# Kernel optimization log

Measured on AMD Instinct MI355X. Metric: run time of the kernel, lower is better.

Reference implementation:

```python
import jax, jax.numpy as jnp
import numpy as np

B, S, P, G, E = 16, 1024, 32, 64, 512
HD = E // 2          # head_dim = 256
SCALE = HD ** -0.5
LAMBDA_INIT = 0.8 - 0.6 * float(np.exp(-0.3 * 0.0))  # depth=0 -> 0.2
EPS = 1e-5


def setup_inputs() -> dict:
    key = jax.random.key(0)
    ks = jax.random.split(key, 12)
    inp = {
        'query': jax.random.normal(ks[0], (B, S, E), jnp.float32),
        'key': jax.random.normal(ks[1], (B, P, G, E), jnp.float32),
        'mask': jax.random.randint(ks[2], (B, S), 0, 2).astype(bool),
        'Wq': jax.random.normal(ks[3], (E, E), jnp.float32) * (E ** -0.5),
        'Wk': jax.random.normal(ks[4], (E, E), jnp.float32) * (E ** -0.5),
        'Wv': jax.random.normal(ks[5], (E, E), jnp.float32) * (E ** -0.5),
        'Wo': jax.random.normal(ks[6], (E, E), jnp.float32) * (E ** -0.5),
        'lq1': jax.random.normal(ks[7], (HD,), jnp.float32) * 0.1,
        'lk1': jax.random.normal(ks[8], (HD,), jnp.float32) * 0.1,
        'lq2': jax.random.normal(ks[9], (HD,), jnp.float32) * 0.1,
        'lk2': jax.random.normal(ks[10], (HD,), jnp.float32) * 0.1,
        'gamma': jnp.ones((E,), jnp.float32),
    }
    return inp


def reference(query, key, mask, Wq, Wk, Wv, Wo, lq1, lk1, lq2, lk2, gamma):
    b, s, e = query.shape
    _, p, g, _ = key.shape
    L = p * g
    key2d = key.reshape(b, L, e)

    Q = (query @ Wq).reshape(b, s, 2, HD).transpose(0, 2, 1, 3) * SCALE  # [B,2,S,hd]
    K = (key2d @ Wk).reshape(b, L, 2, HD).transpose(0, 2, 1, 3)          # [B,2,L,hd]
    V = key2d @ Wv                                                       # [B,L,E]

    scores = jnp.einsum('bhsd,bhld->bhsl', Q, K)                         # [B,2,S,L]
    # masked_fill(~mask, 0.0) with mask broadcast [B,1,S,1]
    scores = jnp.where(mask[:, None, :, None], scores, 0.0)
    attn = jax.nn.softmax(scores, axis=-1)

    lam1 = jnp.exp(jnp.sum(lq1 * lk1))
    lam2 = jnp.exp(jnp.sum(lq2 * lk2))
    lam = lam1 - lam2 + LAMBDA_INIT

    diff = attn[:, 0] - lam * attn[:, 1]                                 # [B,S,L]
    out2d = jnp.einsum('bsl,ble->bse', diff, V)                          # [B,S,E]

    # RMSNorm over last dim with affine gamma
    rms = out2d * jax.lax.rsqrt(jnp.mean(out2d * out2d, axis=-1, keepdims=True) + EPS)
    rms = rms * gamma
    out = (rms * (1.0 - LAMBDA_INIT)) @ Wo                               # [B,S,E]

    return out, diff.reshape(b, s, p, g)
```

## Files before the change

### kernel.cpp

```cpp
#include <hip/hip_runtime.h>
#include <hip/hip_bf16.h>


typedef short short8 __attribute__((ext_vector_type(8)));
typedef __bf16 bf16x8 __attribute__((ext_vector_type(8)));
typedef float f32x4 __attribute__((ext_vector_type(4)));

#define LDS_BYTES 16384
#define OUT0_ELEMS 8388608L

__global__ void probe_kernel(const void* gamma, const void* mask, int* flags)
{
    if (threadIdx.x == 0) {
        unsigned g = *(const unsigned*)gamma;
        flags[0] = (g == 0x3F800000u) ? 1 : 0;
        flags[1] = 0;
    }
    __syncthreads();
    const unsigned* mi = (const unsigned*)mask;
    int bad = 0;
    for (int i = threadIdx.x; i < 4096; i += blockDim.x)
        if (mi[i] > 1u) bad = 1;
    if (bad) atomicOr(&flags[1], 1);
}

__device__ __forceinline__ float read_elem(const void* p, int i, int isf32)
{
    return isf32 ? ((const float*)p)[i]
                 : __bfloat162float(((const __hip_bfloat16*)p)[i]);
}

__global__ void prep_kernel(const void* __restrict__ mask, int* __restrict__ maskI,
                            const void* __restrict__ gamma, float* __restrict__ gammaF,
                            const void* __restrict__ Wq, const void* __restrict__ Wk,
                            const void* __restrict__ Wv, const void* __restrict__ Wo,
                            __hip_bfloat16* __restrict__ WT,
                            const void* __restrict__ lq1, const void* __restrict__ lk1,
                            const void* __restrict__ lq2, const void* __restrict__ lk2,
                            float* __restrict__ lamp, float* __restrict__ lst,
                            const int* __restrict__ flags)
{
    const int bid = blockIdx.x, tid = threadIdx.x;
    const int f = flags[0];
    if (bid < 4096) {
        int which = bid >> 10;
        const void* s = (which == 0) ? Wq : (which == 1) ? Wk : (which == 2) ? Wv : Wo;
        __hip_bfloat16* d = WT + (long)which * 262144;
        int idx = (bid & 1023) * 256 + tid;
        int k = idx >> 9, n = idx & 511;
        d[n * 512 + k] = __float2bfloat16(read_elem(s, idx, f));
    } else if (bid < 4160) {
        int i = (bid - 4096) * 256 + tid;
        if (flags[1]) maskI[i] = ((const unsigned char*)mask)[i] ? 1 : 0;
        else          maskI[i] = ((const int*)mask)[i] ? 1 : 0;
    } else if (bid < 4162) {
        int i = (bid - 4160) * 256 + tid;
        gammaF[i] = read_elem(gamma, i, f);
    } else if (bid < 4290) {
        lst[(bid - 4162) * 256 + tid] = 0.0f;
    } else {
        if (tid < 64) {
            float s1 = 0.0f, s2 = 0.0f;
#pragma unroll
            for (int j = 0; j < 4; ++j) {
                int idx = tid * 4 + j;
                s1 += read_elem(lq1, idx, f) * read_elem(lk1, idx, f);
                s2 += read_elem(lq2, idx, f) * read_elem(lk2, idx, f);
            }
#pragma unroll
            for (int off = 1; off < 64; off <<= 1) {
                s1 += __shfl_xor(s1, off);
                s2 += __shfl_xor(s2, off);
            }
            if (tid == 0) *lamp = __expf(s1) - __expf(s2) + 0.2f;
        }
    }
}

__device__ __forceinline__ void stage_u(const void* A, long aoff, int lda, int af32,
                                        const __hip_bfloat16* B, int ldb,
                                        int kt, char* smem, int tid)
{
    if (af32) {
#pragma unroll
        for (int j = 0; j < 2; ++j) {
            int chunk = j * 256 + tid;
            const float* g = (const float*)A + aoff + (long)(chunk >> 2) * lda + kt + (chunk & 3) * 8;
            f32x4 x0 = *(const f32x4*)g;
            f32x4 x1 = *(const f32x4*)(g + 4);
            __hip_bfloat16 tmp[8];
#pragma unroll
            for (int t = 0; t < 4; ++t) tmp[t] = __float2bfloat16(x0[t]);
#pragma unroll
            for (int t = 0; t < 4; ++t) tmp[4 + t] = __float2bfloat16(x1[t]);
            *(short8*)(smem + chunk * 16) = *(const short8*)tmp;
        }
    } else {
#pragma unroll
        for (int j = 0; j < 2; ++j) {
            int chunk = j * 256 + tid;
            const __hip_bfloat16* g = (const __hip_bfloat16*)A + aoff
                                    + (long)(chunk >> 2) * lda + kt + (chunk & 3) * 8;
            __builtin_amdgcn_global_load_lds(
                (__attribute__((address_space(1))) void*)g,
                (__attribute__((address_space(3))) void*)(smem + chunk * 16), 16, 0, 0);
        }
    }
#pragma unroll
    for (int j = 0; j < 2; ++j) {
        int chunk = j * 256 + tid;
        const __hip_bfloat16* g = B + (long)(chunk >> 2) * ldb + kt + (chunk & 3) * 8;
        __builtin_amdgcn_global_load_lds(
            (__attribute__((address_space(1))) void*)g,
            (__attribute__((address_space(3))) void*)(smem + 8192 + chunk * 16), 16, 0, 0);
    }
}

__device__ __forceinline__ void mfma_block(char* smem, int tid, f32x4 (&acc)[4][4])
{
    const int lane = tid & 63, wid = tid >> 6;
    const int wm = wid >> 1, wn = wid & 1;
    const int lm = lane & 15, lq = lane >> 4;
    short8 a[4], b[4];
#pragma unroll
    for (int i = 0; i < 4; ++i)
        a[i] = *(const short8*)(smem + (wm * 64 + i * 16 + lm) * 64 + lq * 16);
#pragma unroll
    for (int i = 0; i < 4; ++i)
        b[i] = *(const short8*)(smem + 8192 + (wn * 64 + i * 16 + lm) * 64 + lq * 16);
#pragma unroll
    for (int i = 0; i < 4; ++i)
#pragma unroll
        for (int j = 0; j < 4; ++j)
            acc[i][j] = __builtin_amdgcn_mfma_f32_16x16x32_bf16(
                __builtin_bit_cast(bf16x8, a[i]),
                __builtin_bit_cast(bf16x8, b[j]),
                acc[i][j], 0, 0, 0);
}

__device__ __forceinline__ void zero_acc(f32x4 (&acc)[4][4])
{
#pragma unroll
    for (int i = 0; i < 4; ++i)
#pragma unroll
        for (int j = 0; j < 4; ++j)
#pragma unroll
            for (int r = 0; r < 4; ++r) acc[i][j][r] = 0.0f;
}

__device__ __forceinline__ void tile_gemm_u(const void* A, long aoff, int lda, int af32,
                                            const __hip_bfloat16* B, int ldb, int K,
                                            char* smem, int tid, f32x4 (&acc)[4][4])
{
    zero_acc(acc);
    for (int kt = 0; kt < K; kt += 32) {
        __syncthreads();
        stage_u(A, aoff, lda, af32, B, ldb, kt, smem, tid);
        __syncthreads();
        mfma_block(smem, tid, acc);
    }
}

template <int MODE, int AF>
__launch_bounds__(256, 4)
__global__ void gemm_u(const void* __restrict__ A,
                       const __hip_bfloat16* __restrict__ B,
                       void* __restrict__ C,
                       int K, int lda, int ldb, int ldc,
                       long sA, long sB, long sC, float scale,
                       const int* __restrict__ flags)
{
    __shared__ __align__(16) char smem[LDS_BYTES];
    const int tid = threadIdx.x;
    const int bn = blockIdx.x, bm = blockIdx.y, bz = blockIdx.z;
    const int af32 = AF ? flags[0] : 0;
    const long aoff = (long)bz * sA + (long)bm * 128 * lda;
    const __hip_bfloat16* Bb = B + (long)bz * sB + (long)bn * 128 * ldb;

    f32x4 acc[4][4];
    tile_gemm_u(A, aoff, lda, af32, Bb, ldb, K, smem, tid, acc);

    const int f32o = (MODE == 3) ? flags[0] : 0;
    const int lane = tid & 63, wid = tid >> 6;
    const int wm = wid >> 1, wn = wid & 1;
    const int lm = lane & 15, lq = lane >> 4;
#pragma unroll
    for (int im = 0; im < 4; ++im)
#pragma unroll
        for (int in = 0; in < 4; ++in)
#pragma unroll
            for (int r = 0; r < 4; ++r) {
                int row = bm * 128 + wm * 64 + im * 16 + lq * 4 + r;
                int col = bn * 128 + wn * 64 + in * 16 + lm;
                float v = acc[im][in][r] * scale;
                if (MODE == 0) {
                    ((__hip_bfloat16*)C)[bz * sC + (long)row * ldc + col] = __float2bfloat16(v);
                } else if (MODE == 2) {
                    ((float*)C)[bz * sC + (long)row * ldc + col] = v;
                } else if (MODE == 3) {
                    long idx = bz * sC + (long)row * ldc + col;
                    if (f32o) ((float*)C)[idx] = v;
                    else      ((__hip_bfloat16*)C)[idx] = __float2bfloat16(v);
                } else {
                    int bb = row >> 11, l = row & 2047;
                    ((__hip_bfloat16*)C)[((long)bb * 512 + col) * 2048 + l] = __float2bfloat16(v);
                }
            }
}

__launch_bounds__(256, 2)
__global__ void kv_gemm(const void* __restrict__ A,
                        const __hip_bfloat16* __restrict__ Bk,
                        const __hip_bfloat16* __restrict__ Bv,
                        __hip_bfloat16* __restrict__ Kb,
                        __hip_bfloat16* __restrict__ Vt,
                        const int* __restrict__ flags)
{
    __shared__ __align__(16) char smem[24576];
    const int tid = threadIdx.x;
    const int bn = blockIdx.x, bm = blockIdx.y;
    const int af32 = flags[0];
    const long aoff = (long)bm * 128 * 512;
    const __hip_bfloat16* Bkb = Bk + (long)bn * 128 * 512;
    const __hip_bfloat16* Bvb = Bv + (long)bn * 128 * 512;

    f32x4 acck[4][4], accv[4][4];
    zero_acc(acck); zero_acc(accv);

    const int lane = tid & 63, wid = tid >> 6;
    const int wm = wid >> 1, wn = wid & 1;
    const int lm = lane & 15, lq = lane >> 4;

    for (int kt = 0; kt < 512; kt += 32) {
        __syncthreads();
        if (af32) {
#pragma unroll
            for (int j = 0; j < 2; ++j) {
                int chunk = j * 256 + tid;
                const float* g = (const float*)A + aoff + (long)(chunk >> 2) * 512 + kt + (chunk & 3) * 8;
                f32x4 x0 = *(const f32x4*)g;
                f32x4 x1 = *(const f32x4*)(g + 4);
                __hip_bfloat16 tmp[8];
#pragma unroll
                for (int t = 0; t < 4; ++t) tmp[t] = __float2bfloat16(x0[t]);
#pragma unroll
                for (int t = 0; t < 4; ++t) tmp[4 + t] = __float2bfloat16(x1[t]);
                *(short8*)(smem + chunk * 16) = *(const short8*)tmp;
            }
        } else {
#pragma unroll
            for (int j = 0; j < 2; ++j) {
                int chunk = j * 256 + tid;
                const __hip_bfloat16* g = (const __hip_bfloat16*)A + aoff
                                        + (long)(chunk >> 2) * 512 + kt + (chunk & 3) * 8;
                __builtin_amdgcn_global_load_lds(
                    (__attribute__((address_space(1))) void*)g,
                    (__attribute__((address_space(3))) void*)(smem + chunk * 16), 16, 0, 0);
            }
        }
#pragma unroll
        for (int j = 0; j < 2; ++j) {
            int chunk = j * 256 + tid;
            const __hip_bfloat16* gk = Bkb + (long)(chunk >> 2) * 512 + kt + (chunk & 3) * 8;
            __builtin_amdgcn_global_load_lds(
                (__attribute__((address_space(1))) void*)gk,
                (__attribute__((address_space(3))) void*)(smem + 8192 + chunk * 16), 16, 0, 0);
        }
#pragma unroll
        for (int j = 0; j < 2; ++j) {
            int chunk = j * 256 + tid;
            const __hip_bfloat16* gv = Bvb + (long)(chunk >> 2) * 512 + kt + (chunk & 3) * 8;
            __builtin_amdgcn_global_load_lds(
                (__attribute__((address_space(1))) void*)gv,
                (__attribute__((address_space(3))) void*)(smem + 16384 + chunk * 16), 16, 0, 0);
        }
        __syncthreads();
        short8 a[4], bk[4], bv[4];
#pragma unroll
        for (int i = 0; i < 4; ++i)
            a[i] = *(const short8*)(smem + (wm * 64 + i * 16 + lm) * 64 + lq * 16);
#pragma unroll
        for (int i = 0; i < 4; ++i)
            bk[i] = *(const short8*)(smem + 8192 + (wn * 64 + i * 16 + lm) * 64 + lq * 16);
#pragma unroll
        for (int i = 0; i < 4; ++i)
            bv[i] = *(const short8*)(smem + 16384 + (wn * 64 + i * 16 + lm) * 64 + lq * 16);
#pragma unroll
        for (int i = 0; i < 4; ++i)
#pragma unroll
            for (int j = 0; j < 4; ++j) {
                acck[i][j] = __builtin_amdgcn_mfma_f32_16x16x32_bf16(
                    __builtin_bit_cast(bf16x8, a[i]),
                    __builtin_bit_cast(bf16x8, bk[j]),
                    acck[i][j], 0, 0, 0);
                accv[i][j] = __builtin_amdgcn_mfma_f32_16x16x32_bf16(
                    __builtin_bit_cast(bf16x8, a[i]),
                    __builtin_bit_cast(bf16x8, bv[j]),
                    accv[i][j], 0, 0, 0);
            }
    }

#pragma unroll
    for (int im = 0; im < 4; ++im)
#pragma unroll
        for (int in = 0; in < 4; ++in)
#pragma unroll
            for (int r = 0; r < 4; ++r) {
                int row = bm * 128 + wm * 64 + im * 16 + lq * 4 + r;
                int col = bn * 128 + wn * 64 + in * 16 + lm;
                Kb[(long)row * 512 + col] = __float2bfloat16(acck[im][in][r]);
                int bb = row >> 11, l = row & 2047;
                Vt[((long)bb * 512 + col) * 2048 + l] = __float2bfloat16(accv[im][in][r]);
            }
}

__device__ __forceinline__ void score_epilogue(
    f32x4 (&acc)[4][4], char* smem, int tid,
    int nt, int st, int b, int bl, const int* __restrict__ mask,
    float* __restrict__ lstats, __hip_bfloat16* __restrict__ P, int h)
{
    const int lane = tid & 63, wid = tid >> 6;
    const int wm = wid >> 1, wn = wid & 1;
    const int lm = lane & 15, lq = lane >> 4;
    float esum[4][4];
#pragma unroll
    for (int im = 0; im < 4; ++im)
#pragma unroll
        for (int r = 0; r < 4; ++r) {
            int rl = wm * 64 + im * 16 + lq * 4 + r;
            int s  = st * 128 + rl;
            int mv = mask[b * 1024 + s];
            float es = 0.0f;
#pragma unroll
            for (int in = 0; in < 4; ++in) {
                int col = nt * 128 + wn * 64 + in * 16 + lm;
                float sc = mv ? acc[im][in][r] : 0.0f;
                float e  = __expf(sc);
                P[((long)bl * 1024 + s) * 2048 + col] = __float2bfloat16(e);
                float t = e;
                t += __shfl_xor(t, 1);
                t += __shfl_xor(t, 2);
                t += __shfl_xor(t, 4);
                t += __shfl_xor(t, 8);
                es += t;
            }
            esum[im][r] = es;
        }
    __syncthreads();
    float* red = (float*)smem;
    if (lm == 0) {
#pragma unroll
        for (int im = 0; im < 4; ++im)
#pragma unroll
            for (int r = 0; r < 4; ++r)
                red[wn * 128 + wm * 64 + im * 16 + lq * 4 + r] = esum[im][r];
    }
    __syncthreads();
    if (tid < 128)
        atomicAdd(&lstats[((long)(b * 2 + h)) * 1024 + st * 128 + tid],
                  red[tid] + red[128 + tid]);
}

__launch_bounds__(256, 3)
__global__ void score_kernel(const __hip_bfloat16* __restrict__ Q,
                             const __hip_bfloat16* __restrict__ Km,
                             const int* __restrict__ mask,
                             float* __restrict__ lstats,
                             __hip_bfloat16* __restrict__ P0,
                             __hip_bfloat16* __restrict__ P1,
                             int bbase)
{
    __shared__ __align__(16) char smem[LDS_BYTES];
    const int tid = threadIdx.x;
    const int nt = blockIdx.x, st = blockIdx.y, bl = blockIdx.z;
    const int b = bl + bbase;
    const long A0 = ((long)b * 1024 + st * 128) * 512;
    const __hip_bfloat16* B0 = Km + ((long)b * 2048 + nt * 128) * 512;

    f32x4 acc[4][4];
    tile_gemm_u(Q, A0, 512, 0, B0, 512, 256, smem, tid, acc);
    score_epilogue(acc, smem, tid, nt, st, b, bl, mask, lstats, P0, 0);
    tile_gemm_u(Q, A0 + 256, 512, 0, B0 + 256, 512, 256, smem, tid, acc);
    score_epilogue(acc, smem, tid, nt, st, b, bl, mask, lstats, P1, 1);
}

__global__ void finalize_kernel(__hip_bfloat16* P0,
                                const __hip_bfloat16* __restrict__ P1,
                                const float* __restrict__ lstats,
                                const float* __restrict__ lamp,
                                void* dout, int bbase,
                                const int* __restrict__ flags)
{
    const long row = blockIdx.x;
    const int bl = (int)(row >> 10), s = (int)(row & 1023);
    const int b  = bl + bbase;
    const int tid = threadIdx.x;
    const float lam = *lamp;
    const float i0 = 1.0f / lstats[((long)(b * 2)) * 1024 + s];
    const float i1 = lam  / lstats[((long)(b * 2 + 1)) * 1024 + s];
    const long lbase = row * 2048 + (long)tid * 8;

    union { short8 v; __hip_bfloat16 h[8]; } u0, u1, ub;
    u0.v = *(const short8*)(P0 + lbase);
    u1.v = *(const short8*)(P1 + lbase);
    float d[8];
#pragma unroll
    for (int j = 0; j < 8; ++j)
        d[j] = __bfloat162float(u0.h[j]) * i0 - __bfloat162float(u1.h[j]) * i1;

    const long gidx = ((long)b * 1024 + s) * 2048 + (long)tid * 8;
    if (flags[0]) {
        float* outF = (float*)dout + OUT0_ELEMS;
        f32x4 v0, v1;
#pragma unroll
        for (int j = 0; j < 4; ++j) { v0[j] = d[j]; v1[j] = d[4 + j]; }
        *(f32x4*)(outF + gidx)     = v0;
        *(f32x4*)(outF + gidx + 4) = v1;
    } else {
        __hip_bfloat16* outH = (__hip_bfloat16*)dout + OUT0_ELEMS;
        union { short8 v; __hip_bfloat16 h[8]; } uo;
#pragma unroll
        for (int j = 0; j < 8; ++j) uo.h[j] = __float2bfloat16(d[j]);
        *(short8*)(outH + gidx) = uo.v;
    }
#pragma unroll
    for (int j = 0; j < 8; ++j) ub.h[j] = __float2bfloat16(d[j]);
    *(short8*)(P0 + lbase) = ub.v;
}

__global__ void rmsnorm_kernel(const float* __restrict__ X,
                               const float* __restrict__ gamma,
                               __hip_bfloat16* __restrict__ Y)
{
    long row = blockIdx.x;
    int lane = threadIdx.x;
    const float* x = X + row * 512 + lane * 8;
    f32x4 v0 = *(const f32x4*)x;
    f32x4 v1 = *(const f32x4*)(x + 4);
    float ss = v0[0] * v0[0] + v0[1] * v0[1] + v0[2] * v0[2] + v0[3] * v0[3]
             + v1[0] * v1[0] + v1[1] * v1[1] + v1[2] * v1[2] + v1[3] * v1[3];
#pragma unroll
    for (int off = 1; off < 64; off <<= 1) ss += __shfl_xor(ss, off);
    float rinv = rsqrtf(ss * (1.0f / 512.0f) + 1e-5f) * 0.8f;
#pragma unroll
    for (int j = 0; j < 4; ++j)
        Y[row * 512 + lane * 8 + j] = __float2bfloat16(v0[j] * rinv * gamma[lane * 8 + j]);
#pragma unroll
    for (int j = 0; j < 4; ++j)
        Y[row * 512 + lane * 8 + 4 + j] = __float2bfloat16(v1[j] * rinv * gamma[lane * 8 + 4 + j]);
}

extern "C" void kernel_launch(void* const* d_in, const int* in_sizes, int n_in,
                              void* d_out, int out_size, void* d_ws, size_t ws_size,
                              hipStream_t stream)
{
    const void* query = d_in[0];
    const void* key2d = d_in[1];
    const void* maskp = d_in[2];
    const void* Wq    = d_in[3];
    const void* Wk    = d_in[4];
    const void* Wv    = d_in[5];
    const void* Wo    = d_in[6];
    const void* lq1   = d_in[7];
    const void* lk1   = d_in[8];
    const void* lq2   = d_in[9];
    const void* lk2   = d_in[10];
    const void* gamma = d_in[11];

    char* w = (char*)d_ws;
    __hip_bfloat16* WT    = (__hip_bfloat16*)(w);
    __hip_bfloat16* WqT   = WT;
    __hip_bfloat16* WkT   = WT + 262144;
    __hip_bfloat16* WvT   = WT + 524288;
    __hip_bfloat16* WoT   = WT + 786432;
    float*          lamp  = (float*)(w + 2097152);
    int*            flags = (int*)(w + 2097216);
    float*          gammaF= (float*)(w + 2097280);
    int*            maskI = (int*)(w + 2162688);
    __hip_bfloat16* Qb    = (__hip_bfloat16*)(w + 2228224);
    __hip_bfloat16* Kb    = (__hip_bfloat16*)(w + 19005440);
    __hip_bfloat16* Vt    = (__hip_bfloat16*)(w + 52559872);
    float*          lst   = (float*)(w + 86114304);
    float*          o2d   = (float*)(w + 86245376);
    __hip_bfloat16* rmsb  = (__hip_bfloat16*)(w + 119799808);
    __hip_bfloat16* diffBF= (__hip_bfloat16*)(w + 136577024);
    __hip_bfloat16* P1s   = (__hip_bfloat16*)(w + 103022592);

    const bool hugews = ws_size >= 270794752UL;
    const bool bigws  = ws_size >= 203685888UL;

    probe_kernel<<<1, 256, 0, stream>>>(gamma, maskp, flags);
    prep_kernel<<<4291, 256, 0, stream>>>(maskp, maskI, gamma, gammaF,
        Wq, Wk, Wv, Wo, WT, lq1, lk1, lq2, lk2, lamp, lst, flags);

    gemm_u<0, 1><<<dim3(4, 128, 1), 256, 0, stream>>>(query, WqT, Qb,
        512, 512, 512, 512, 0, 0, 0, 0.0625f, flags);
    kv_gemm<<<dim3(4, 256), 256, 0, stream>>>(key2d, WkT, WvT, Kb, Vt, flags);

    if (hugews) {
        __hip_bfloat16* P0f = diffBF;
        __hip_bfloat16* P1f = diffBF + 33554432L;
        score_kernel<<<dim3(16, 8, 16), 256, 0, stream>>>(Qb, Kb, maskI, lst,
            P0f, P1f, 0);
        finalize_kernel<<<16384, 256, 0, stream>>>(P0f, P1f, lst, lamp,
            d_out, 0, flags);
        gemm_u<2, 0><<<dim3(4, 8, 16), 256, 0, stream>>>(P0f, Vt, o2d,
            2048, 2048, 2048, 512, 1024L * 2048, 512L * 2048, 1024L * 512, 1.0f, flags);
    } else if (bigws) {
        __hip_bfloat16* P0h = diffBF;
        __hip_bfloat16* P1h = diffBF + 16777216L;
        for (int h = 0; h < 2; ++h) {
            int bb = h * 8;
            score_kernel<<<dim3(16, 8, 8), 256, 0, stream>>>(Qb, Kb, maskI, lst,
                P0h, P1h, bb);
            finalize_kernel<<<8192, 256, 0, stream>>>(P0h, P1h, lst, lamp,
                d_out, bb, flags);
            gemm_u<2, 0><<<dim3(4, 8, 8), 256, 0, stream>>>(P0h,
                Vt + (long)bb * 512 * 2048, o2d + (long)bb * 1024 * 512,
                2048, 2048, 2048, 512, 1024L * 2048, 512L * 2048, 1024L * 512, 1.0f, flags);
        }
    } else {
        __hip_bfloat16* scratch = (__hip_bfloat16*)d_out;
        for (int h = 0; h < 2; ++h) {
            int bb = h * 8;
            score_kernel<<<dim3(16, 8, 8), 256, 0, stream>>>(Qb, Kb, maskI, lst,
                scratch, P1s, bb);
            finalize_kernel<<<8192, 256, 0, stream>>>(scratch, P1s, lst, lamp,
                d_out, bb, flags);
            gemm_u<2, 0><<<dim3(4, 8, 8), 256, 0, stream>>>(scratch,
                Vt + (long)bb * 512 * 2048, o2d + (long)bb * 1024 * 512,
                2048, 2048, 2048, 512, 1024L * 2048, 512L * 2048, 1024L * 512, 1.0f, flags);
        }
    }

    rmsnorm_kernel<<<16384, 64, 0, stream>>>(o2d, gammaF, rmsb);

    gemm_u<3, 0><<<dim3(4, 128, 1), 256, 0, stream>>>(rmsb, WoT, d_out,
        512, 512, 512, 512, 0, 0, 1024L * 512, 1.0f, flags);
}
```

Baseline: 629.0 us.

## Widen score kernel tile to 128x256 with direct global-to-LDS loads

```diff
diff --git a/kernel.cpp b/kernel.cpp
--- a/kernel.cpp
+++ b/kernel.cpp
@@ -314,54 +314,7 @@
             }
 }
 
-__device__ __forceinline__ void score_epilogue(
-    f32x4 (&acc)[4][4], char* smem, int tid,
-    int nt, int st, int b, int bl, const int* __restrict__ mask,
-    float* __restrict__ lstats, __hip_bfloat16* __restrict__ P, int h)
-{
-    const int lane = tid & 63, wid = tid >> 6;
-    const int wm = wid >> 1, wn = wid & 1;
-    const int lm = lane & 15, lq = lane >> 4;
-    float esum[4][4];
-#pragma unroll
-    for (int im = 0; im < 4; ++im)
-#pragma unroll
-        for (int r = 0; r < 4; ++r) {
-            int rl = wm * 64 + im * 16 + lq * 4 + r;
-            int s  = st * 128 + rl;
-            int mv = mask[b * 1024 + s];
-            float es = 0.0f;
-#pragma unroll
-            for (int in = 0; in < 4; ++in) {
-                int col = nt * 128 + wn * 64 + in * 16 + lm;
-                float sc = mv ? acc[im][in][r] : 0.0f;
-                float e  = __expf(sc);
-                P[((long)bl * 1024 + s) * 2048 + col] = __float2bfloat16(e);
-                float t = e;
-                t += __shfl_xor(t, 1);
-                t += __shfl_xor(t, 2);
-                t += __shfl_xor(t, 4);
-                t += __shfl_xor(t, 8);
-                es += t;
-            }
-            esum[im][r] = es;
-        }
-    __syncthreads();
-    float* red = (float*)smem;
-    if (lm == 0) {
-#pragma unroll
-        for (int im = 0; im < 4; ++im)
-#pragma unroll
-            for (int r = 0; r < 4; ++r)
-                red[wn * 128 + wm * 64 + im * 16 + lq * 4 + r] = esum[im][r];
-    }
-    __syncthreads();
-    if (tid < 128)
-        atomicAdd(&lstats[((long)(b * 2 + h)) * 1024 + st * 128 + tid],
-                  red[tid] + red[128 + tid]);
-}
-
-__launch_bounds__(256, 3)
+__launch_bounds__(256, 2)
 __global__ void score_kernel(const __hip_bfloat16* __restrict__ Q,
                              const __hip_bfloat16* __restrict__ Km,
                              const int* __restrict__ mask,
@@ -370,18 +323,94 @@
                              __hip_bfloat16* __restrict__ P1,
                              int bbase)
 {
-    __shared__ __align__(16) char smem[LDS_BYTES];
+    __shared__ __align__(16) char smem[26624];
     const int tid = threadIdx.x;
     const int nt = blockIdx.x, st = blockIdx.y, bl = blockIdx.z;
     const int b = bl + bbase;
-    const long A0 = ((long)b * 1024 + st * 128) * 512;
-    const __hip_bfloat16* B0 = Km + ((long)b * 2048 + nt * 128) * 512;
-
-    f32x4 acc[4][4];
-    tile_gemm_u(Q, A0, 512, 0, B0, 512, 256, smem, tid, acc);
-    score_epilogue(acc, smem, tid, nt, st, b, bl, mask, lstats, P0, 0);
-    tile_gemm_u(Q, A0 + 256, 512, 0, B0 + 256, 512, 256, smem, tid, acc);
-    score_epilogue(acc, smem, tid, nt, st, b, bl, mask, lstats, P1, 1);
+    const __hip_bfloat16* Abase = Q + ((long)b * 1024 + st * 128) * 512;
+    const __hip_bfloat16* Bbase = Km + ((long)b * 2048 + nt * 256) * 512;
+    float* red = (float*)(smem + 24576);
+
+    const int lane = tid & 63, wid = tid >> 6;
+    const int lm = lane & 15, lq = lane >> 4;
+
+#pragma unroll
+    for (int h = 0; h < 2; ++h) {
+        const __hip_bfloat16* Ap = Abase + h * 256;
+        const __hip_bfloat16* Bp = Bbase + h * 256;
+        __hip_bfloat16* P = h ? P1 : P0;
+
+        f32x4 acc[8][4];
+#pragma unroll
+        for (int i = 0; i < 8; ++i)
+#pragma unroll
+            for (int j = 0; j < 4; ++j)
+#pragma unroll
+                for (int r = 0; r < 4; ++r) acc[i][j][r] = 0.0f;
+
+        for (int kt = 0; kt < 256; kt += 32) {
+            __syncthreads();
+#pragma unroll
+            for (int j = 0; j < 2; ++j) {
+                int c = j * 256 + tid;
+                const __hip_bfloat16* g = Ap + (long)(c >> 2) * 512 + kt + (c & 3) * 8;
+                __builtin_amdgcn_global_load_lds(
+                    (__attribute__((address_space(1))) void*)g,
+                    (__attribute__((address_space(3))) void*)(smem + c * 16), 16, 0, 0);
+            }
+#pragma unroll
+            for (int j = 0; j < 4; ++j) {
+                int c = j * 256 + tid;
+                const __hip_bfloat16* g = Bp + (long)(c >> 2) * 512 + kt + (c & 3) * 8;
+                __builtin_amdgcn_global_load_lds(
+                    (__attribute__((address_space(1))) void*)g,
+                    (__attribute__((address_space(3))) void*)(smem + 8192 + c * 16), 16, 0, 0);
+            }
+            __syncthreads();
+            short8 a[8], bf[4];
+#pragma unroll
+            for (int i = 0; i < 8; ++i)
+                a[i] = *(const short8*)(smem + (i * 16 + lm) * 64 + lq * 16);
+#pragma unroll
+            for (int j = 0; j < 4; ++j)
+                bf[j] = *(const short8*)(smem + 8192 + (wid * 64 + j * 16 + lm) * 64 + lq * 16);
+#pragma unroll
+            for (int i = 0; i < 8; ++i)
+#pragma unroll
+                for (int j = 0; j < 4; ++j)
+                    acc[i][j] = __builtin_amdgcn_mfma_f32_16x16x32_bf16(
+                        __builtin_bit_cast(bf16x8, a[i]),
+                        __builtin_bit_cast(bf16x8, bf[j]),
+                        acc[i][j], 0, 0, 0);
+        }
+
+#pragma unroll
+        for (int im = 0; im < 8; ++im)
+#pragma unroll
+            for (int r = 0; r < 4; ++r) {
+                int rl = im * 16 + lq * 4 + r;
+                int s  = st * 128 + rl;
+                int mv = mask[b * 1024 + s];
+                float es = 0.0f;
+#pragma unroll
+                for (int in = 0; in < 4; ++in) {
+                    int col = nt * 256 + wid * 64 + in * 16 + lm;
+                    float sc = mv ? acc[im][in][r] : 0.0f;
+                    float e  = __expf(sc);
+                    P[((long)bl * 1024 + s) * 2048 + col] = __float2bfloat16(e);
+                    es += e;
+                }
+                es += __shfl_xor(es, 1);
+                es += __shfl_xor(es, 2);
+                es += __shfl_xor(es, 4);
+                es += __shfl_xor(es, 8);
+                if (lm == 0) red[wid * 128 + rl] = es;
+            }
+        __syncthreads();
+        if (tid < 128)
+            atomicAdd(&lstats[((long)(b * 2 + h)) * 1024 + st * 128 + tid],
+                      red[tid] + red[128 + tid] + red[256 + tid] + red[384 + tid]);
+    }
 }
 
 __global__ void finalize_kernel(__hip_bfloat16* P0,
@@ -500,7 +529,7 @@
     if (hugews) {
         __hip_bfloat16* P0f = diffBF;
         __hip_bfloat16* P1f = diffBF + 33554432L;
-        score_kernel<<<dim3(16, 8, 16), 256, 0, stream>>>(Qb, Kb, maskI, lst,
+        score_kernel<<<dim3(8, 8, 16), 256, 0, stream>>>(Qb, Kb, maskI, lst,
             P0f, P1f, 0);
         finalize_kernel<<<16384, 256, 0, stream>>>(P0f, P1f, lst, lamp,
             d_out, 0, flags);
@@ -511,7 +540,7 @@
         __hip_bfloat16* P1h = diffBF + 16777216L;
         for (int h = 0; h < 2; ++h) {
             int bb = h * 8;
-            score_kernel<<<dim3(16, 8, 8), 256, 0, stream>>>(Qb, Kb, maskI, lst,
+            score_kernel<<<dim3(8, 8, 8), 256, 0, stream>>>(Qb, Kb, maskI, lst,
                 P0h, P1h, bb);
             finalize_kernel<<<8192, 256, 0, stream>>>(P0h, P1h, lst, lamp,
                 d_out, bb, flags);
@@ -523,7 +552,7 @@
         __hip_bfloat16* scratch = (__hip_bfloat16*)d_out;
         for (int h = 0; h < 2; ++h) {
             int bb = h * 8;
-            score_kernel<<<dim3(16, 8, 8), 256, 0, stream>>>(Qb, Kb, maskI, lst,
+            score_kernel<<<dim3(8, 8, 8), 256, 0, stream>>>(Qb, Kb, maskI, lst,
                 scratch, P1s, bb);
             finalize_kernel<<<8192, 256, 0, stream>>>(scratch, P1s, lst, lamp,
                 d_out, bb, flags);
```

New measurement: 627.3 us. Within noise of the previous version (-0.3%).
